# Kernel tuning notes

Measured on AMD Instinct MI355X. Metric: run time of the kernel, lower is better.

Reference implementation:

```python
import jax, jax.numpy as jnp
import numpy as np

LN_EPS = 1e-5

def setup_inputs() -> dict:
    key = jax.random.key(0)
    k1, k2, k3 = jax.random.split(key, 3)
    L, B, D = 2048, 8, 1024
    x = jax.random.normal(k1, (L, B, D), dtype=jnp.float32)
    c = jnp.zeros((B, D), dtype=jnp.float32)
    W = jax.random.normal(k2, (D, 3 * D), dtype=jnp.float32) * 0.02
    # bias init from _init_bias: u-bias 0, f-bias 0.5, r-bias 0
    b = jnp.concatenate([jnp.zeros(D), jnp.full((D,), 0.5), jnp.zeros(D)]).astype(jnp.float32)
    gamma = jnp.ones((D,), dtype=jnp.float32)
    beta = jnp.zeros((D,), dtype=jnp.float32)
    return {"x": x, "c": c, "W": W, "b": b, "gamma": gamma, "beta": beta}

def reference(x, c, W, b, gamma, beta):
    # LayerNorm over last dim
    mu = jnp.mean(x, axis=-1, keepdims=True)
    var = jnp.mean(jnp.square(x - mu), axis=-1, keepdims=True)
    x_norm = (x - mu) * jax.lax.rsqrt(var + LN_EPS) * gamma + beta
    # Fused u/f/r projection: [L,B,3D]
    ufr = jnp.einsum('lbd,de->lbe', x_norm, W) + b
    u, f, r = jnp.split(ufr, 3, axis=-1)
    f_gate = jax.nn.sigmoid(f)
    r_gate = jax.nn.sigmoid(r)
    # Linear recurrence c_t = f_t * c_{t-1} + (1-f_t) * u_t via scan over time
    def step(c_prev, fu):
        f_t, u_t = fu
        c_t = f_t * c_prev + (1.0 - f_t) * u_t
        return c_t, c_t
    last_c, c_stack = jax.lax.scan(step, c, (f_gate, u))
    hs = r_gate * jnp.tanh(c_stack) + (1.0 - r_gate) * x_norm
    return x + hs, last_c
```

## Files before the change

### kernel.cpp

```cpp
#include <hip/hip_runtime.h>
#include <hip/hip_bf16.h>


typedef unsigned short u16;
typedef __bf16 bf16x8 __attribute__((ext_vector_type(8)));
typedef float f32x4 __attribute__((ext_vector_type(4)));

#define L_DIM 2048
#define B_DIM 8
#define D_DIM 1024
#define M_DIM (L_DIM * B_DIM)
#define K_DIM D_DIM
#define N_DIM (3 * D_DIM)
#define NCH 32
#define CLEN (L_DIM / NCH)
#define NT 16
#define NREP 3
#define GTOT (NT * NREP)

#define LDS_A 0
#define LDS_B 65536
#define LDS_DUMMY 131072
#define LDS_TOTAL 147456

__device__ __forceinline__ float bf2f(u16 h) {
    unsigned int u = ((unsigned int)h) << 16;
    float f;
    __builtin_memcpy(&f, &u, 4);
    return f;
}

__device__ __forceinline__ u16 f2bf(float f) {
    unsigned int u;
    __builtin_memcpy(&u, &f, 4);
    u = u + 0x7fff + ((u >> 16) & 1);
    return (u16)(u >> 16);
}

__device__ __forceinline__ void async16(void* lds, const void* g) {
    __builtin_amdgcn_global_load_lds(
        (const __attribute__((address_space(1))) void*)g,
        (__attribute__((address_space(3))) void*)lds, 16, 0, 0);
}

__global__ __launch_bounds__(256) void ln_kernel(const float* __restrict__ x,
                                                 const float* __restrict__ gamma,
                                                 const float* __restrict__ beta,
                                                 u16* __restrict__ xn,
                                                 float2* __restrict__ mrs) {
    int row = blockIdx.x;
    int tid = threadIdx.x;
    const float4* xr = (const float4*)(x + (size_t)row * D_DIM);
    float4 v = xr[tid];
    float s = v.x + v.y + v.z + v.w;
    float q = v.x * v.x + v.y * v.y + v.z * v.z + v.w * v.w;
    #pragma unroll
    for (int off = 32; off; off >>= 1) {
        s += __shfl_down(s, off);
        q += __shfl_down(q, off);
    }
    __shared__ float ss[4], qq[4];
    int lane = tid & 63, wv = tid >> 6;
    if (lane == 0) { ss[wv] = s; qq[wv] = q; }
    __syncthreads();
    s = ss[0] + ss[1] + ss[2] + ss[3];
    q = qq[0] + qq[1] + qq[2] + qq[3];
    float mu = s * (1.0f / D_DIM);
    float var = q * (1.0f / D_DIM) - mu * mu;
    float rs = rsqrtf(var + 1e-5f);
    if (tid == 0) mrs[row] = make_float2(mu, rs);
    float4 g = ((const float4*)gamma)[tid];
    float4 bt = ((const float4*)beta)[tid];
    ushort4 o;
    o.x = f2bf((v.x - mu) * rs * g.x + bt.x);
    o.y = f2bf((v.y - mu) * rs * g.y + bt.y);
    o.z = f2bf((v.z - mu) * rs * g.z + bt.z);
    o.w = f2bf((v.w - mu) * rs * g.w + bt.w);
    ((ushort4*)(xn + (size_t)row * D_DIM))[tid] = o;
}

__global__ __launch_bounds__(256) void wt_kernel(const float* __restrict__ W,
                                                 u16* __restrict__ Wt) {
    __shared__ float t[64][65];
    int k0 = blockIdx.x * 64;
    int n0 = blockIdx.y * 64;
    int col = threadIdx.x & 63;
    int rg4 = threadIdx.x >> 6;
    #pragma unroll
    for (int j = 0; j < 16; ++j) {
        int r = rg4 * 16 + j;
        t[r][col] = W[(size_t)(k0 + r) * N_DIM + n0 + col];
    }
    __syncthreads();
    #pragma unroll
    for (int j = 0; j < 16; ++j) {
        int nr = rg4 * 16 + j;
        Wt[(size_t)(n0 + nr) * K_DIM + k0 + col] = f2bf(t[col][nr]);
    }
}

__global__ __launch_bounds__(512, 2) void gemm_kernel(const u16* __restrict__ A,
                                                      const u16* __restrict__ Bt,
                                                      const float* __restrict__ bias,
                                                      u16* __restrict__ uo,
                                                      u16* __restrict__ fo,
                                                      u16* __restrict__ ro) {
    extern __shared__ char lds[];
    const int tid = threadIdx.x;
    const int wave = tid >> 6, lane = tid & 63;
    const int lm = lane & 15, lg = lane >> 4;
    const int wm = wave >> 2, wn = wave & 3;
    const int bid = blockIdx.x;
    const int m0 = (bid & 63) * 256;
    const int n0base = (bid >> 6) * 768;

    const int c0 = tid, c1 = 512 + tid;
    const int r0 = c0 >> 3, cc0 = (c0 & 7) ^ (r0 & 7);
    const int r1 = c1 >> 3, cc1 = (c1 & 7) ^ (r1 & 7);
    const char* gA0 = (const char*)A + ((size_t)(m0 + r0) * K_DIM + cc0 * 8) * 2;
    const char* gA1 = (const char*)A + ((size_t)(m0 + r1) * K_DIM + cc1 * 8) * 2;
    const int boB0 = (r0 * K_DIM + cc0 * 8) * 2;
    const int boB1 = (r1 * K_DIM + cc1 * 8) * 2;
    char* dstBase = lds + wave * 1024;

    f32x4 acc[8][4];
    bf16x8 av[4][2], bv[4][2];

    auto stageA = [&](int g1, int h) {
        char* dst = (g1 < GTOT) ? (dstBase + (g1 & 1) * 32768 + h * 16384)
                                : (lds + LDS_DUMMY + wave * 1024);
        int kb = ((g1 & 15) << 7) + (h << 18);
        async16(dst,        gA0 + kb);
        async16(dst + 8192, gA1 + kb);
    };
    auto stageB = [&](int g2, int h) {
        char* dst = (g2 < GTOT) ? (dstBase + LDS_B + (g2 & 1) * 32768 + h * 16384)
                                : (lds + LDS_DUMMY + wave * 1024);
        int gc = (g2 < GTOT) ? g2 : 0;
        const char* src = (const char*)Bt
            + (size_t)(n0base + (gc >> 4) * 256) * (K_DIM * 2)
            + ((gc & 15) << 7) + (h << 18);
        async16(dst,        src + boB0);
        async16(dst + 8192, src + boB1);
    };

#define LDA(bb, mf0)                                                            \
    do { _Pragma("unroll")                                                      \
        for (int q = 0; q < 4; ++q) {                                           \
            int row_ = wm * 128 + ((mf0) + q) * 16 + lm;                        \
            const char* p_ = lds + LDS_A + (bb) * 32768 + row_ * 128;           \
            _Pragma("unroll")                                                   \
            for (int kk = 0; kk < 2; ++kk)                                      \
                av[q][kk] = *(const bf16x8*)(p_ + ((((kk << 2) | lg) ^ (lm & 7)) << 4)); \
        } } while (0)

#define LDB(bb, kk)                                                             \
    do { _Pragma("unroll")                                                      \
        for (int nf = 0; nf < 4; ++nf) {                                        \
            int row_ = wn * 64 + nf * 16 + lm;                                  \
            bv[nf][kk] = *(const bf16x8*)(lds + LDS_B + (bb) * 32768 + row_ * 128 \
                                          + ((((kk << 2) | lg) ^ (lm & 7)) << 4)); \
        } } while (0)

#define MFMA16(r0q, kk)                                                         \
    do { _Pragma("unroll")                                                      \
        for (int q = 0; q < 4; ++q)                                             \
            _Pragma("unroll")                                                   \
            for (int nf = 0; nf < 4; ++nf)                                      \
                acc[(r0q) + q][nf] = __builtin_amdgcn_mfma_f32_16x16x32_bf16(   \
                    av[q][kk], bv[nf][kk], acc[(r0q) + q][nf], 0, 0, 0);        \
    } while (0)

#define PH_SYNC()                                                               \
    do { __builtin_amdgcn_s_barrier();                                          \
         asm volatile("s_waitcnt lgkmcnt(0)");                                  \
         __builtin_amdgcn_sched_barrier(0); } while (0)

#define TILE_BODY(g, bb)                                                        \
    do {                                                                        \
        LDA(bb, 0);                                                             \
        LDB(bb, 0);                                                             \
        stageA((g) + 1, 0);                                                     \
        PH_SYNC();                                                              \
        __builtin_amdgcn_s_setprio(1);  MFMA16(0, 0);                           \
        __builtin_amdgcn_s_setprio(0);  __builtin_amdgcn_s_barrier();           \
        LDB(bb, 1);                                                             \
        stageA((g) + 1, 1);                                                     \
        PH_SYNC();                                                              \
        __builtin_amdgcn_s_setprio(1);  MFMA16(0, 1);                           \
        __builtin_amdgcn_s_setprio(0);  __builtin_amdgcn_s_barrier();           \
        LDA(bb, 4);                                                             \
        stageB((g) + 2, 0);                                                     \
        PH_SYNC();                                                              \
        __builtin_amdgcn_s_setprio(1);  MFMA16(4, 0);                           \
        __builtin_amdgcn_s_setprio(0);  __builtin_amdgcn_s_barrier();           \
        stageB((g) + 2, 1);                                                     \
        __builtin_amdgcn_s_barrier();                                           \
        __builtin_amdgcn_s_setprio(1);  MFMA16(4, 1);                           \
        __builtin_amdgcn_s_setprio(0);                                          \
        asm volatile("s_waitcnt vmcnt(4)" ::: "memory");                        \
        __builtin_amdgcn_s_barrier();                                           \
    } while (0)

    stageA(0, 0); stageA(0, 1);
    stageB(0, 0); stageB(0, 1);
    stageB(1, 0); stageB(1, 1);
    asm volatile("s_waitcnt vmcnt(4)" ::: "memory");
    __builtin_amdgcn_s_barrier();

    #pragma unroll 1
    for (int rep = 0; rep < NREP; ++rep) {
        #pragma unroll
        for (int i = 0; i < 8; ++i)
            #pragma unroll
            for (int j = 0; j < 4; ++j)
                acc[i][j] = (f32x4){0.f, 0.f, 0.f, 0.f};
        const int gbase = rep * NT;
        #pragma unroll 1
        for (int t = 0; t < NT; t += 2) {
            TILE_BODY(gbase + t, 0);
            TILE_BODY(gbase + t + 1, 1);
        }
        int n0 = n0base + rep * 256;
        int seg = n0 >> 10;
        u16* outp = (seg == 0) ? uo : ((seg == 1) ? fo : ro);
        #pragma unroll
        for (int nf = 0; nf < 4; ++nf) {
            int col = n0 + wn * 64 + nf * 16 + lm;
            int cm = col & 1023;
            float bb2 = bias[col];
            #pragma unroll
            for (int mf = 0; mf < 8; ++mf) {
                #pragma unroll
                for (int j = 0; j < 4; ++j) {
                    int row = m0 + wm * 128 + mf * 16 + lg * 4 + j;
                    float val = acc[mf][nf][j] + bb2;
                    if (seg != 0) val = 1.0f / (1.0f + __expf(-val));
                    outp[(size_t)row * D_DIM + cm] = f2bf(val);
                }
            }
        }
    }
#undef LDA
#undef LDB
#undef MFMA16
#undef PH_SYNC
#undef TILE_BODY
}

__global__ __launch_bounds__(256) void scan1_kernel(const u16* __restrict__ fg,
                                                    const u16* __restrict__ u,
                                                    float* __restrict__ Aa,
                                                    float* __restrict__ Ss) {
    int ch = blockIdx.x;
    int bd = (blockIdx.y * 256 + threadIdx.x) * 2;
    int b = bd >> 10, d = bd & 1023;
    float a0 = 1.0f, a1 = 1.0f, s0 = 0.0f, s1 = 0.0f;
    for (int t = ch * CLEN; t < ch * CLEN + CLEN; ++t) {
        size_t idx = ((size_t)(t * B_DIM + b) << 10) + d;
        ushort2 f2 = *(const ushort2*)(fg + idx);
        ushort2 u2 = *(const ushort2*)(u + idx);
        float f0 = bf2f(f2.x), f1 = bf2f(f2.y);
        float v0 = bf2f(u2.x), v1 = bf2f(u2.y);
        s0 = f0 * s0 + (1.0f - f0) * v0;
        s1 = f1 * s1 + (1.0f - f1) * v1;
        a0 *= f0;
        a1 *= f1;
    }
    int o = ch * 8192 + bd;
    *(float2*)(Aa + o) = make_float2(a0, a1);
    *(float2*)(Ss + o) = make_float2(s0, s1);
}

__global__ __launch_bounds__(256) void scan2_kernel(const float* __restrict__ Aa,
                                                    const float* __restrict__ Ss,
                                                    const float* __restrict__ c0,
                                                    float* __restrict__ cs,
                                                    float* __restrict__ lastc) {
    int bd = blockIdx.x * 256 + threadIdx.x;
    float c = c0[bd];
    #pragma unroll 4
    for (int ch = 0; ch < NCH; ++ch) {
        cs[ch * 8192 + bd] = c;
        c = Aa[ch * 8192 + bd] * c + Ss[ch * 8192 + bd];
    }
    lastc[bd] = c;
}

__global__ __launch_bounds__(256) void scan3_kernel(const float* __restrict__ cs,
                                                    const u16* __restrict__ fg,
                                                    const u16* __restrict__ u,
                                                    const u16* __restrict__ rg,
                                                    const float2* __restrict__ mrs,
                                                    const float* __restrict__ gamma,
                                                    const float* __restrict__ beta,
                                                    const float* __restrict__ x,
                                                    float* __restrict__ out) {
    int ch = blockIdx.x;
    int bd = (blockIdx.y * 256 + threadIdx.x) * 2;
    int b = bd >> 10, d = bd & 1023;
    float2 gm = *(const float2*)(gamma + d);
    float2 bt = *(const float2*)(beta + d);
    float c0v = cs[ch * 8192 + bd];
    float c1v = cs[ch * 8192 + bd + 1];
    for (int t = ch * CLEN; t < ch * CLEN + CLEN; ++t) {
        size_t idx = ((size_t)(t * B_DIM + b) << 10) + d;
        ushort2 f2 = *(const ushort2*)(fg + idx);
        ushort2 u2 = *(const ushort2*)(u + idx);
        ushort2 r2 = *(const ushort2*)(rg + idx);
        float2 x2 = *(const float2*)(x + idx);
        float2 mr = mrs[t * B_DIM + b];
        float f0 = bf2f(f2.x), f1 = bf2f(f2.y);
        float v0 = bf2f(u2.x), v1 = bf2f(u2.y);
        float r0 = bf2f(r2.x), r1 = bf2f(r2.y);
        float n0 = (x2.x - mr.x) * mr.y * gm.x + bt.x;
        float n1 = (x2.y - mr.x) * mr.y * gm.y + bt.y;
        c0v = f0 * c0v + (1.0f - f0) * v0;
        c1v = f1 * c1v + (1.0f - f1) * v1;
        float h0 = r0 * tanhf(c0v) + (1.0f - r0) * n0;
        float h1 = r1 * tanhf(c1v) + (1.0f - r1) * n1;
        *(float2*)(out + idx) = make_float2(x2.x + h0, x2.y + h1);
    }
}

extern "C" void kernel_launch(void* const* d_in, const int* in_sizes, int n_in,
                              void* d_out, int out_size, void* d_ws, size_t ws_size,
                              hipStream_t stream) {
    const float* x     = (const float*)d_in[0];
    const float* c0    = (const float*)d_in[1];
    const float* W     = (const float*)d_in[2];
    const float* b     = (const float*)d_in[3];
    const float* gamma = (const float*)d_in[4];
    const float* beta  = (const float*)d_in[5];
    float* out = (float*)d_out;
    float* lastc = out + (size_t)M_DIM * D_DIM;

    char* w = (char*)d_ws;
    u16* xn = (u16*)w;  w += (size_t)M_DIM * D_DIM * 2;
    u16* Wt = (u16*)w;  w += (size_t)N_DIM * K_DIM * 2;
    u16* ug = (u16*)w;  w += (size_t)M_DIM * D_DIM * 2;
    u16* fg = (u16*)w;  w += (size_t)M_DIM * D_DIM * 2;
    u16* rg = (u16*)w;  w += (size_t)M_DIM * D_DIM * 2;
    float* Aa = (float*)w; w += (size_t)NCH * 8192 * 4;
    float* Ss = (float*)w; w += (size_t)NCH * 8192 * 4;
    float* cs = (float*)w; w += (size_t)NCH * 8192 * 4;
    float2* mrs = (float2*)w; w += (size_t)M_DIM * 8;

    hipFuncSetAttribute(reinterpret_cast<const void*>(gemm_kernel),
                        hipFuncAttributeMaxDynamicSharedMemorySize, LDS_TOTAL);

    ln_kernel<<<M_DIM, 256, 0, stream>>>(x, gamma, beta, xn, mrs);
    wt_kernel<<<dim3(K_DIM / 64, N_DIM / 64), 256, 0, stream>>>(W, Wt);
    gemm_kernel<<<256, 512, LDS_TOTAL, stream>>>(xn, Wt, b, ug, fg, rg);
    scan1_kernel<<<dim3(NCH, 16), 256, 0, stream>>>(fg, ug, Aa, Ss);
    scan2_kernel<<<32, 256, 0, stream>>>(Aa, Ss, c0, cs, lastc);
    scan3_kernel<<<dim3(NCH, 16), 256, 0, stream>>>(cs, fg, ug, rg, mrs, gamma, beta, x, out);
}
```

Baseline: 233.2 us.

## Split GEMM into one 256x256 tile per block over a 2D grid

Before, the GEMM ran 256 persistent-style blocks, each looping over three N tiles with the A tile reloaded every time. Now it launches a 64x12 grid where each block computes a single 256x256 output tile, which gives more parallelism and better load balance across CUs. The LDS fragment addressing is also precomputed into per-wave base pointers, and the A/B fragment loads are regrouped into separate registers per k-half so the phases are symmetric. The cost is more block launches and prologue/epilogue overhead, with the A tile fetched separately by each of the 12 column blocks.

New measurement: 215.2 us. 1.08x faster.

```diff
diff --git a/kernel.cpp b/kernel.cpp
--- a/kernel.cpp
+++ b/kernel.cpp
@@ -14,11 +14,8 @@
 #define N_DIM (3 * D_DIM)
 #define NCH 32
 #define CLEN (L_DIM / NCH)
-#define NT 16
-#define NREP 3
-#define GTOT (NT * NREP)
-
-#define LDS_A 0
+#define NT (K_DIM / 64)
+
 #define LDS_B 65536
 #define LDS_DUMMY 131072
 #define LDS_TOTAL 147456
@@ -110,65 +107,62 @@
     const int wave = tid >> 6, lane = tid & 63;
     const int lm = lane & 15, lg = lane >> 4;
     const int wm = wave >> 2, wn = wave & 3;
-    const int bid = blockIdx.x;
-    const int m0 = (bid & 63) * 256;
-    const int n0base = (bid >> 6) * 768;
-
-    const int c0 = tid, c1 = 512 + tid;
-    const int r0 = c0 >> 3, cc0 = (c0 & 7) ^ (r0 & 7);
+    const int m0 = blockIdx.x * 256;
+    const int n0 = blockIdx.y * 256;
+
+    const int xk0 = ((0 | lg) ^ (lm & 7)) << 4;
+    const int xk1 = ((4 | lg) ^ (lm & 7)) << 4;
+    const char* pA0 = lds + (wm * 128 + lm) * 128 + xk0;
+    const char* pA1 = lds + (wm * 128 + lm) * 128 + xk1;
+    const char* pB0 = lds + LDS_B + (wn * 64 + lm) * 128 + xk0;
+    const char* pB1 = lds + LDS_B + (wn * 64 + lm) * 128 + xk1;
+
+    const int c1 = 512 + tid;
+    const int r0 = tid >> 3, cc0 = (tid & 7) ^ (r0 & 7);
     const int r1 = c1 >> 3, cc1 = (c1 & 7) ^ (r1 & 7);
     const char* gA0 = (const char*)A + ((size_t)(m0 + r0) * K_DIM + cc0 * 8) * 2;
     const char* gA1 = (const char*)A + ((size_t)(m0 + r1) * K_DIM + cc1 * 8) * 2;
-    const int boB0 = (r0 * K_DIM + cc0 * 8) * 2;
-    const int boB1 = (r1 * K_DIM + cc1 * 8) * 2;
-    char* dstBase = lds + wave * 1024;
-
-    f32x4 acc[8][4];
-    bf16x8 av[4][2], bv[4][2];
-
-    auto stageA = [&](int g1, int h) {
-        char* dst = (g1 < GTOT) ? (dstBase + (g1 & 1) * 32768 + h * 16384)
-                                : (lds + LDS_DUMMY + wave * 1024);
-        int kb = ((g1 & 15) << 7) + (h << 18);
-        async16(dst,        gA0 + kb);
-        async16(dst + 8192, gA1 + kb);
+    const char* gB0 = (const char*)Bt + ((size_t)(n0 + r0) * K_DIM + cc0 * 8) * 2;
+    const char* gB1 = (const char*)Bt + ((size_t)(n0 + r1) * K_DIM + cc1 * 8) * 2;
+    char* dstW = lds + wave * 1024;
+
+    f32x4 acc[8][4] = {};
+    bf16x8 av[4], aw[4], bv0[4], bv1[4];
+
+    auto stageA = [&](int t1, int h) {
+        char* dst = (t1 < NT) ? (dstW + ((t1 & 1) << 15) + (h << 14))
+                              : (lds + LDS_DUMMY + wave * 1024);
+        int ko = ((t1 & 15) << 7) + (h << 18);
+        async16(dst,        gA0 + ko);
+        async16(dst + 8192, gA1 + ko);
     };
-    auto stageB = [&](int g2, int h) {
-        char* dst = (g2 < GTOT) ? (dstBase + LDS_B + (g2 & 1) * 32768 + h * 16384)
-                                : (lds + LDS_DUMMY + wave * 1024);
-        int gc = (g2 < GTOT) ? g2 : 0;
-        const char* src = (const char*)Bt
-            + (size_t)(n0base + (gc >> 4) * 256) * (K_DIM * 2)
-            + ((gc & 15) << 7) + (h << 18);
-        async16(dst,        src + boB0);
-        async16(dst + 8192, src + boB1);
+    auto stageB = [&](int t2, int h) {
+        char* dst = (t2 < NT) ? (dstW + LDS_B + ((t2 & 1) << 15) + (h << 14))
+                              : (lds + LDS_DUMMY + wave * 1024);
+        int ko = ((t2 & 15) << 7) + (h << 18);
+        async16(dst,        gB0 + ko);
+        async16(dst + 8192, gB1 + ko);
     };
 
-#define LDA(bb, mf0)                                                            \
+#define LDA(dst, pbase, bb, mf0)                                                \
     do { _Pragma("unroll")                                                      \
-        for (int q = 0; q < 4; ++q) {                                           \
-            int row_ = wm * 128 + ((mf0) + q) * 16 + lm;                        \
-            const char* p_ = lds + LDS_A + (bb) * 32768 + row_ * 128;           \
-            _Pragma("unroll")                                                   \
-            for (int kk = 0; kk < 2; ++kk)                                      \
-                av[q][kk] = *(const bf16x8*)(p_ + ((((kk << 2) | lg) ^ (lm & 7)) << 4)); \
-        } } while (0)
-
-#define LDB(bb, kk)                                                             \
+        for (int q = 0; q < 4; ++q)                                             \
+            dst[q] = *(const bf16x8*)(pbase + (bb) * 32768 + ((mf0) + q) * 2048); \
+    } while (0)
+
+#define LDB(dst, pbase, bb)                                                     \
     do { _Pragma("unroll")                                                      \
-        for (int nf = 0; nf < 4; ++nf) {                                        \
-            int row_ = wn * 64 + nf * 16 + lm;                                  \
-            bv[nf][kk] = *(const bf16x8*)(lds + LDS_B + (bb) * 32768 + row_ * 128 \
-                                          + ((((kk << 2) | lg) ^ (lm & 7)) << 4)); \
-        } } while (0)
-
-#define MFMA16(r0q, kk)                                                         \
+        for (int nf = 0; nf < 4; ++nf)                                          \
+            dst[nf] = *(const bf16x8*)(pbase + (bb) * 32768 + nf * 2048);       \
+    } while (0)
+
+#define MFMA16(r0q, afr, bfr)                                                   \
     do { _Pragma("unroll")                                                      \
         for (int q = 0; q < 4; ++q)                                             \
             _Pragma("unroll")                                                   \
             for (int nf = 0; nf < 4; ++nf)                                      \
                 acc[(r0q) + q][nf] = __builtin_amdgcn_mfma_f32_16x16x32_bf16(   \
-                    av[q][kk], bv[nf][kk], acc[(r0q) + q][nf], 0, 0, 0);        \
+                    afr[q], bfr[nf], acc[(r0q) + q][nf], 0, 0, 0);              \
     } while (0)
 
 #define PH_SYNC()                                                               \
@@ -176,27 +170,33 @@
          asm volatile("s_waitcnt lgkmcnt(0)");                                  \
          __builtin_amdgcn_sched_barrier(0); } while (0)
 
-#define TILE_BODY(g, bb)                                                        \
+#define TILE_BODY(t, bb)                                                        \
     do {                                                                        \
-        LDA(bb, 0);                                                             \
-        LDB(bb, 0);                                                             \
-        stageA((g) + 1, 0);                                                     \
+                                                                   \
+        LDA(av, pA0, bb, 0);                                                    \
+        LDB(bv0, pB0, bb);                                                      \
+        stageA((t) + 1, 0);                                                     \
         PH_SYNC();                                                              \
-        __builtin_amdgcn_s_setprio(1);  MFMA16(0, 0);                           \
+        __builtin_amdgcn_s_setprio(1);  MFMA16(0, av, bv0);                     \
         __builtin_amdgcn_s_setprio(0);  __builtin_amdgcn_s_barrier();           \
-        LDB(bb, 1);                                                             \
-        stageA((g) + 1, 1);                                                     \
+                                                                   \
+        LDA(av, pA1, bb, 0);                                                    \
+        LDB(bv1, pB1, bb);                                                      \
+        stageA((t) + 1, 1);                                                     \
         PH_SYNC();                                                              \
-        __builtin_amdgcn_s_setprio(1);  MFMA16(0, 1);                           \
+        __builtin_amdgcn_s_setprio(1);  MFMA16(0, av, bv1);                     \
         __builtin_amdgcn_s_setprio(0);  __builtin_amdgcn_s_barrier();           \
-        LDA(bb, 4);                                                             \
-        stageB((g) + 2, 0);                                                     \
+                                                                   \
+        LDA(aw, pA0, bb, 4);                                                    \
+        stageB((t) + 2, 0);                                                     \
         PH_SYNC();                                                              \
-        __builtin_amdgcn_s_setprio(1);  MFMA16(4, 0);                           \
+        __builtin_amdgcn_s_setprio(1);  MFMA16(4, aw, bv0);                     \
         __builtin_amdgcn_s_setprio(0);  __builtin_amdgcn_s_barrier();           \
-        stageB((g) + 2, 1);                                                     \
-        __builtin_amdgcn_s_barrier();                                           \
-        __builtin_amdgcn_s_setprio(1);  MFMA16(4, 1);                           \
+                                                                   \
+        LDA(aw, pA1, bb, 4);                                                    \
+        stageB((t) + 2, 1);                                                     \
+        PH_SYNC();                                                              \
+        __builtin_amdgcn_s_setprio(1);  MFMA16(4, aw, bv1);                     \
         __builtin_amdgcn_s_setprio(0);                                          \
         asm volatile("s_waitcnt vmcnt(4)" ::: "memory");                        \
         __builtin_amdgcn_s_barrier();                                           \
@@ -208,36 +208,26 @@
     asm volatile("s_waitcnt vmcnt(4)" ::: "memory");
     __builtin_amdgcn_s_barrier();
 
-    #pragma unroll 1
-    for (int rep = 0; rep < NREP; ++rep) {
+    for (int t = 0; t < NT; t += 2) {
+        TILE_BODY(t, 0);
+        TILE_BODY(t + 1, 1);
+    }
+
+    int seg = n0 >> 10;
+    u16* outp = (seg == 0) ? uo : ((seg == 1) ? fo : ro);
+    #pragma unroll
+    for (int nf = 0; nf < 4; ++nf) {
+        int col = n0 + wn * 64 + nf * 16 + lm;
+        int cm = col & 1023;
+        float bb2 = bias[col];
         #pragma unroll
-        for (int i = 0; i < 8; ++i)
+        for (int mf = 0; mf < 8; ++mf) {
             #pragma unroll
-            for (int j = 0; j < 4; ++j)
-                acc[i][j] = (f32x4){0.f, 0.f, 0.f, 0.f};
-        const int gbase = rep * NT;
-        #pragma unroll 1
-        for (int t = 0; t < NT; t += 2) {
-            TILE_BODY(gbase + t, 0);
-            TILE_BODY(gbase + t + 1, 1);
-        }
-        int n0 = n0base + rep * 256;
-        int seg = n0 >> 10;
-        u16* outp = (seg == 0) ? uo : ((seg == 1) ? fo : ro);
-        #pragma unroll
-        for (int nf = 0; nf < 4; ++nf) {
-            int col = n0 + wn * 64 + nf * 16 + lm;
-            int cm = col & 1023;
-            float bb2 = bias[col];
-            #pragma unroll
-            for (int mf = 0; mf < 8; ++mf) {
-                #pragma unroll
-                for (int j = 0; j < 4; ++j) {
-                    int row = m0 + wm * 128 + mf * 16 + lg * 4 + j;
-                    float val = acc[mf][nf][j] + bb2;
-                    if (seg != 0) val = 1.0f / (1.0f + __expf(-val));
-                    outp[(size_t)row * D_DIM + cm] = f2bf(val);
-                }
+            for (int j = 0; j < 4; ++j) {
+                int row = m0 + wm * 128 + mf * 16 + lg * 4 + j;
+                float val = acc[mf][nf][j] + bb2;
+                if (seg != 0) val = 1.0f / (1.0f + __expf(-val));
+                outp[(size_t)row * D_DIM + cm] = f2bf(val);
             }
         }
     }
@@ -351,7 +341,7 @@
 
     ln_kernel<<<M_DIM, 256, 0, stream>>>(x, gamma, beta, xn, mrs);
     wt_kernel<<<dim3(K_DIM / 64, N_DIM / 64), 256, 0, stream>>>(W, Wt);
-    gemm_kernel<<<256, 512, LDS_TOTAL, stream>>>(xn, Wt, b, ug, fg, rg);
+    gemm_kernel<<<dim3(M_DIM / 256, N_DIM / 256), 512, LDS_TOTAL, stream>>>(xn, Wt, b, ug, fg, rg);
     scan1_kernel<<<dim3(NCH, 16), 256, 0, stream>>>(fg, ug, Aa, Ss);
     scan2_kernel<<<32, 256, 0, stream>>>(Aa, Ss, c0, cs, lastc);
     scan3_kernel<<<dim3(NCH, 16), 256, 0, stream>>>(cs, fg, ug, rg, mrs, gamma, beta, x, out);
```
